# Kernel tuning notes

Measured on AMD Instinct MI355X. Metric: run time of the kernel, lower is better.

Reference implementation:

```python
import jax, jax.numpy as jnp
import numpy as np
from jax import lax

KS = 7  # kernel-prediction footprint at 1/4 res
DN = ('NCHW', 'OIHW', 'NCHW')


def _conv(x, W, b):
    y = lax.conv_general_dilated(x, W, (1, 1), 'VALID', dimension_numbers=DN)
    return y + b[None, :, None, None]


def _apply_kernels(kernel, data, ks):
    # kernel: [bs, ks*ks, kh, kw]; data: [bs, 1, h, w]
    kh, kw = kernel.shape[2], kernel.shape[3]
    h, w = data.shape[2], data.shape[3]
    ch = (h - (kh + ks - 1)) // 2
    cw = (w - (kw + ks - 1)) // 2
    if ch > 0:
        data = data[:, :, ch:h - ch, :]
    if cw > 0:
        data = data[:, :, :, cw:w - cw]
    # patches: [bs, ks*ks, kh, kw], flat tap index = dy*ks+dx (row-major), same as torch unfold+view
    patches = lax.conv_general_dilated_patches(data, (ks, ks), (1, 1), 'VALID')
    return jnp.sum(kernel * patches, axis=1, keepdims=True)


def _crop_like(a, b):
    dh = (a.shape[2] - b.shape[2]) // 2
    dw = (a.shape[3] - b.shape[3]) // 2
    if dh > 0 or dw > 0:
        a = a[:, :, dh:a.shape[2] - dh, dw:a.shape[3] - dw]
    return a


def _unroll(buf):
    # [bs,4,h,w] quarter-res -> [bs,1,2h,2w] full-res (channel c=2p+q -> offset (p,q))
    bs, _, h, w = buf.shape
    return buf.reshape(bs, 2, 2, h, w).transpose(0, 3, 1, 4, 2).reshape(bs, 1, 2 * h, 2 * w)


def reference(mosaic, W0, b0, W1, b1, W2, b2, W3, b3, W4, b4):
    gray = mosaic.sum(axis=1)  # [bs,H,W]
    # GRBG 2x2 phase extraction, matching torch unfold(2,2,2).unfold(1,2,2).permute(0,3,4,1,2)
    g0 = gray[:, 0::2, 0::2][:, None]
    b_ = gray[:, 1::2, 0::2][:, None]
    r = gray[:, 0::2, 1::2][:, None]
    g1 = gray[:, 1::2, 1::2][:, None]
    x = jnp.concatenate([g0, b_, r, g1], axis=1)  # [bs,4,h,w]

    # ConvChain: 5 valid 3x3 convs, relu on all but last (linear output)
    for (W, bb) in ((W0, b0), (W1, b1), (W2, b2), (W3, b3)):
        x = jax.nn.relu(_conv(x, W, bb))
    kernels = _conv(x, W4, b4)  # [bs, 10*KS*KS, kh, kw]

    k2 = KS * KS
    idx = 0

    reds = [r]
    for _ in range(3):
        k = jax.nn.softmax(kernels[:, idx:idx + k2], axis=1)
        idx += k2
        reds.append(_apply_kernels(k, r, KS))
    reds[0] = _crop_like(reds[0], reds[1])
    red = _unroll(jnp.concatenate([reds[1], reds[0], reds[2], reds[3]], axis=1))

    blues = [b_]
    for _ in range(3):
        k = jax.nn.softmax(kernels[:, idx:idx + k2], axis=1)
        idx += k2
        blues.append(_apply_kernels(k, b_, KS))
    blues[0] = _crop_like(blues[0], blues[1])
    blue = _unroll(jnp.concatenate([blues[1], blues[2], blues[0], blues[3]], axis=1))

    greens = [g0, g1]
    for _ in range(2):
        k = jax.nn.softmax(kernels[:, idx:idx + 2 * k2], axis=1)
        idx += 2 * k2
        greens.append(_apply_kernels(k[:, :k2], g0, KS) + _apply_kernels(k[:, k2:], g1, KS))
    greens[0] = _crop_like(greens[0], greens[2])
    greens[1] = _crop_like(greens[1], greens[2])
    green = _unroll(jnp.concatenate([greens[0], greens[2], greens[3], greens[1]], axis=1))

    return jnp.concatenate([red, green, blue], axis=1)  # [bs,3,2*kh,2*kw]


def setup_inputs() -> dict:
    key = jax.random.key(0)
    ks = jax.random.split(key, 6)
    bs, H, W = 2, 768, 768
    mosaic = jax.random.uniform(ks[0], (bs, 3, H, W), dtype=jnp.float32)

    def w(k, o, i):
        return jax.random.normal(k, (o, i, 3, 3), jnp.float32) * (1.0 / np.sqrt(i * 9))

    z = lambda n: jnp.zeros((n,), jnp.float32)
    return {
        'mosaic': mosaic,
        'W0': w(ks[1], 64, 4), 'b0': z(64),
        'W1': w(ks[2], 64, 64), 'b1': z(64),
        'W2': w(ks[3], 64, 64), 'b2': z(64),
        'W3': w(ks[4], 64, 64), 'b3': z(64),
        'W4': w(ks[5], 490, 64), 'b4': z(490),
    }
```

## Files before the change

### kernel.cpp

```cpp
#include <hip/hip_runtime.h>
#include <hip/hip_bf16.h>
#include <math.h>


typedef __attribute__((ext_vector_type(8))) short short8;
typedef __attribute__((ext_vector_type(4))) short short4v;
typedef __attribute__((ext_vector_type(4))) float f32x4;

static __device__ __forceinline__ short f2bf(float v) {
    __bf16 h = (__bf16)v;
    return __builtin_bit_cast(short, h);
}

__global__ __launch_bounds__(256) void split_k(const float* __restrict__ mosaic,
                                               float* __restrict__ x0) {
    int idx = blockIdx.x * 256 + threadIdx.x;
    const int total = 2 * 4 * 384 * 384;
    if (idx >= total) return;
    int x = idx % 384;
    int t = idx / 384;
    int y = t % 384;  t /= 384;
    int c = t % 4;
    int b = t / 4;
    int Y = 2 * y + ((c == 1 || c == 3) ? 1 : 0);
    int X = 2 * x + ((c == 2 || c == 3) ? 1 : 0);
    const float* mb = mosaic + (size_t)b * 3 * 768 * 768;
    float g = mb[Y * 768 + X] + mb[768 * 768 + Y * 768 + X] + mb[2 * 768 * 768 + Y * 768 + X];
    x0[idx] = g;
}

__global__ __launch_bounds__(256) void repack_k(const float* __restrict__ W,
                                                short* __restrict__ dst) {
    int idx = blockIdx.x * 256 + threadIdx.x;
    if (idx >= 9 * 64 * 64) return;
    int ic = idx % 64;
    int t2 = idx / 64;
    int oc = t2 % 64;
    int t  = t2 / 64;
    dst[idx] = f2bf(W[((size_t)oc * 64 + ic) * 9 + t]);
}

__global__ __launch_bounds__(256) void repack4_k(const float* __restrict__ W4,
                                                 const float* __restrict__ b4,
                                                 short* __restrict__ Wq,
                                                 float* __restrict__ bq) {
    int idx = blockIdx.x * 256 + threadIdx.x;
    if (idx < 9 * 640 * 64) {
        int ic  = idx % 64;
        int t2  = idx / 64;
        int ocn = t2 % 640;
        int tap = t2 / 640;
        int k  = ocn >> 6;
        int ql = ocn & 63;
        float v = (ql < 49) ? W4[((size_t)(49 * k + ql) * 64 + ic) * 9 + tap] : 0.f;
        Wq[idx] = f2bf(v);
    }
    if (idx < 640) {
        int k = idx >> 6, ql = idx & 63;
        bq[idx] = (ql < 49) ? b4[49 * k + ql] : 0.f;
    }
}

__global__ __launch_bounds__(256) void conv0_k(const float* __restrict__ x0f,
                                               const float* __restrict__ W0,
                                               const float* __restrict__ b0,
                                               short* __restrict__ out) {
    __shared__ float w[64 * 36];
    __shared__ float bb[64];
    for (int e = threadIdx.x; e < 64 * 36; e += 256) w[e] = W0[e];
    if (threadIdx.x < 64) bb[threadIdx.x] = b0[threadIdx.x];
    __syncthreads();
    int idx = blockIdx.x * 256 + threadIdx.x;
    if (idx >= 2 * 382 * 382) return;
    int x = idx % 382;
    int t = idx / 382;
    int y = t % 382;
    int b = t / 382;
    const float* base = x0f + (size_t)b * 4 * 384 * 384;
    float in[4][9];
#pragma unroll
    for (int ic = 0; ic < 4; ++ic)
#pragma unroll
        for (int ky = 0; ky < 3; ++ky)
#pragma unroll
            for (int kx = 0; kx < 3; ++kx)
                in[ic][ky * 3 + kx] = base[ic * 384 * 384 + (y + ky) * 384 + (x + kx)];
    short* op = out + (((size_t)b * 382 + y) * 382 + x) * 64;
    float accs[8];
    for (int og = 0; og < 8; ++og) {
#pragma unroll
        for (int oo = 0; oo < 8; ++oo) {
            int oc = og * 8 + oo;
            float acc = bb[oc];
            const float* wp = w + oc * 36;
#pragma unroll
            for (int ic = 0; ic < 4; ++ic)
#pragma unroll
                for (int e = 0; e < 9; ++e)
                    acc = fmaf(in[ic][e], wp[ic * 9 + e], acc);
            accs[oo] = fmaxf(acc, 0.f);
        }
        short8 pk;
#pragma unroll
        for (int oo = 0; oo < 8; ++oo) pk[oo] = f2bf(accs[oo]);
        *(short8*)(op + og * 8) = pk;
    }
}

template <int EPI>
__global__ __launch_bounds__(256, 2) void convp_k(
    const short* __restrict__ act,
    int Hin, int Hout, int YITER, int nstrips,
    const short* __restrict__ Wq,
    int CoutT,
    const float* __restrict__ bias,
    short* __restrict__ outbf,
    const float* __restrict__ x0f,
    float* __restrict__ out,
    float* __restrict__ pM, float* __restrict__ pD, float* __restrict__ pN) {
    const int tid = threadIdx.x;
    const int wave = tid >> 6;
    const int lane = tid & 63;
    const int wr = wave >> 1, wc = wave & 1;
    const int l15 = lane & 15, l4 = lane >> 4;

    const int q8 = gridDim.x >> 3;
    int L = ((int)blockIdx.x & 7) * q8 + ((int)blockIdx.x >> 3);
    int z = 0;
    if (EPI) { z = L % 10; L /= 10; }
    const int xt = L % 6; L /= 6;
    const int strip = L % nstrips;
    const int b = L / nstrips;
    const int x0c = xt * 64;
    const int y0 = strip * YITER;
    const int cnt = min(YITER, Hout - y0);
    if (cnt <= 0) return;

    __shared__ __align__(16) short Bt[8 * 528 * 8];
    __shared__ float smM[2][64], smD[2][64], smN[2][64];
    __shared__ float smP[17 * 72];

    auto stage_row = [&](int r) {
        const size_t rowbase = ((size_t)b * Hin + r) * (size_t)Hin;
        const int ring = (r & 7) * 528;
#pragma unroll
        for (int i = 0; i < 2; ++i) {
            int s = i * 256 + tid;
            int xl = s >> 3, sl = s & 7;
            int gx = x0c + xl; if (gx > Hin - 1) gx = Hin - 1;
            const short* src = act + (rowbase + gx) * 64 + ((sl ^ (xl & 7)) << 3);
            __builtin_amdgcn_global_load_lds(
                (const __attribute__((address_space(1))) void*)src,
                (__attribute__((address_space(3))) void*)((char*)Bt + (ring + s) * 16),
                16, 0, 0);
        }
        if (tid < 16) {
            int s = 512 + tid;
            int xl = s >> 3, sl = s & 7;
            int gx = x0c + xl; if (gx > Hin - 1) gx = Hin - 1;
            const short* src = act + (rowbase + gx) * 64 + ((sl ^ (xl & 7)) << 3);
            __builtin_amdgcn_global_load_lds(
                (const __attribute__((address_space(1))) void*)src,
                (__attribute__((address_space(3))) void*)((char*)Bt + (ring + s) * 16),
                16, 0, 0);
        }
    };

    const int zrow = EPI ? z * 64 : 0;
    short8 wreg[9][2][2];
#pragma unroll
    for (int tap = 0; tap < 9; ++tap)
#pragma unroll
        for (int kk = 0; kk < 2; ++kk)
#pragma unroll
            for (int m = 0; m < 2; ++m)
                wreg[tap][kk][m] = *(const short8*)(Wq +
                    ((size_t)tap * CoutT + zrow + wr * 32 + m * 16 + l15) * 64
                    + kk * 32 + l4 * 8);

    float bv[2][4];
    int goff[2][4];
    if (EPI) {
        int pidx = (z < 3) ? 2 : (z < 6) ? 1 : ((z & 1) ? 3 : 0);
        const float* plane = x0f + ((size_t)b * 4 + pidx) * 384 * 384;
#pragma unroll
        for (int m = 0; m < 2; ++m)
#pragma unroll
            for (int r = 0; r < 4; ++r) {
                int q = wr * 32 + m * 16 + l4 * 4 + r;
                bv[m][r] = (q < 49) ? bias[z * 64 + q] : -1e30f;
                int qc = (q < 49) ? q : 48;
                goff[m][r] = (qc / 7) * 72 + (qc % 7);
            }
        for (int e = tid; e < 17 * 70; e += 256) {
            int pr = e / 70, pc = e % 70;
            int gy = y0 + 2 + pr; if (gy > 383) gy = 383;
            int gx = x0c + 2 + pc; if (gx > 383) gx = 383;
            smP[pr * 72 + pc] = plane[gy * 384 + gx];
        }
    }

    stage_row(y0);
    stage_row(y0 + 1);
    stage_row(y0 + 2);
    stage_row(y0 + 3);
    stage_row(y0 + 4);
    asm volatile("s_waitcnt vmcnt(4) lgkmcnt(0)\n\ts_barrier" ::: "memory");

    for (int i = 0; i < cnt; ++i) {
        const int y = y0 + i;

        f32x4 acc[2][2] = {};
#pragma unroll
        for (int tap = 0; tap < 9; ++tap) {
            const int ky = tap / 3, kx = tap % 3;
            const int rbase = ((y + ky) & 7) * 528;
            short8 bf[2][2];
#pragma unroll
            for (int kk = 0; kk < 2; ++kk)
#pragma unroll
                for (int n = 0; n < 2; ++n) {
                    int xl = wc * 32 + n * 16 + l15 + kx;
                    int slot = (kk * 4 + l4) ^ (xl & 7);
                    bf[kk][n] = *(const short8*)&Bt[(rbase + xl * 8 + slot) * 8];
                }
#pragma unroll
            for (int kk = 0; kk < 2; ++kk)
#pragma unroll
                for (int m = 0; m < 2; ++m)
#pragma unroll
                    for (int n = 0; n < 2; ++n)
                        acc[m][n] = __builtin_amdgcn_mfma_f32_16x16x32_bf16(
                            wreg[tap][kk][m], bf[kk][n], acc[m][n], 0, 0, 0);
        }

        if (!EPI) {
#pragma unroll
            for (int m = 0; m < 2; ++m) {
                int ocb = wr * 32 + m * 16 + l4 * 4;
#pragma unroll
                for (int n = 0; n < 2; ++n) {
                    int x = x0c + wc * 32 + n * 16 + l15;
                    if (x >= Hout) continue;
                    size_t off = (((size_t)b * Hout + y) * Hout + x) * 64 + ocb;
                    short4v pk;
#pragma unroll
                    for (int r = 0; r < 4; ++r)
                        pk[r] = f2bf(fmaxf(acc[m][n][r] + bias[ocb + r], 0.f));
                    *(short4v*)(outbf + off) = pk;
                }
            }
        } else {
#pragma unroll
            for (int n = 0; n < 2; ++n) {
                const int xn = x0c + wc * 32 + n * 16 + l15;
                const int xg = (xn < 374) ? xn : 373;
                const int gbase = i * 72 + (xg - x0c);
                float mx = -1e30f;
#pragma unroll
                for (int m = 0; m < 2; ++m)
#pragma unroll
                    for (int r = 0; r < 4; ++r)
                        mx = fmaxf(mx, acc[m][n][r] + bv[m][r]);
                mx = fmaxf(mx, __shfl_xor(mx, 16));
                mx = fmaxf(mx, __shfl_xor(mx, 32));
                float den = 0.f, num = 0.f;
#pragma unroll
                for (int m = 0; m < 2; ++m)
#pragma unroll
                    for (int r = 0; r < 4; ++r) {
                        float e = __expf(acc[m][n][r] + bv[m][r] - mx);
                        den += e;
                        num = fmaf(e, smP[gbase + goff[m][r]], num);
                    }
                den += __shfl_xor(den, 16);  den += __shfl_xor(den, 32);
                num += __shfl_xor(num, 16);  num += __shfl_xor(num, 32);
                if (l4 == 0) {
                    int p = wc * 32 + n * 16 + l15;
                    smM[wr][p] = mx;
                    smD[wr][p] = den;
                    smN[wr][p] = num;
                }
            }
            asm volatile("s_waitcnt lgkmcnt(0)\n\ts_barrier" ::: "memory");
            if (tid < 64) {
                int p = tid, x = x0c + p;
                if (x < 374) {
                    float m0 = smM[0][p], m1 = smM[1][p];
                    float M = fmaxf(m0, m1);
                    float s0 = __expf(m0 - M), s1 = __expf(m1 - M);
                    float D = smD[0][p] * s0 + smD[1][p] * s1;
                    float N = smN[0][p] * s0 + smN[1][p] * s1;
                    if (z < 6) {
                        int color = (z < 3) ? 0 : 2;
                        int oy, ox;
                        switch (z) {
                            case 0: oy = 0; ox = 0; break;
                            case 1: oy = 1; ox = 0; break;
                            case 2: oy = 1; ox = 1; break;
                            case 3: oy = 0; ox = 0; break;
                            case 4: oy = 0; ox = 1; break;
                            default: oy = 1; ox = 1; break;
                        }
                        out[(((size_t)b * 3 + color) * 748 + 2 * y + oy) * 748 + 2 * x + ox] = N / D;
                    } else {
                        size_t po = (((size_t)(z - 6) * 2 + b) * 374 + y) * 374 + x;
                        pM[po] = M; pD[po] = D; pN[po] = N;
                    }
                }
            }
        }

        if (i <= cnt - 4) stage_row(y + 5);
        asm volatile("s_waitcnt vmcnt(4) lgkmcnt(0)\n\ts_barrier" ::: "memory");
    }
}

__global__ __launch_bounds__(256) void rawcomb_k(
    const float* __restrict__ x0f,
    const float* __restrict__ pM, const float* __restrict__ pD,
    const float* __restrict__ pN,
    float* __restrict__ out) {
    int idx = blockIdx.x * 256 + threadIdx.x;
    if (idx >= 2 * 374 * 374) return;
    int x = idx % 374;
    int t = idx / 374;
    int y = t % 374;
    int b = t / 374;
    const float* pb = x0f + (size_t)b * 4 * 384 * 384;
    float* ob = out + (size_t)b * 3 * 748 * 748;
    float g0v = pb[(y + 5) * 384 + x + 5];
    float blv = pb[384 * 384 + (y + 5) * 384 + x + 5];
    float rrv = pb[2 * 384 * 384 + (y + 5) * 384 + x + 5];
    float g1v = pb[3 * 384 * 384 + (y + 5) * 384 + x + 5];
    ob[((size_t)0 * 748 + 2 * y) * 748 + 2 * x + 1]     = rrv;
    ob[((size_t)2 * 748 + 2 * y + 1) * 748 + 2 * x]     = blv;
    ob[((size_t)1 * 748 + 2 * y) * 748 + 2 * x]         = g0v;
    ob[((size_t)1 * 748 + 2 * y + 1) * 748 + 2 * x + 1] = g1v;
#pragma unroll
    for (int g = 0; g < 2; ++g) {
        size_t o0 = (((size_t)(g * 2 + 0) * 2 + b) * 374 + y) * 374 + x;
        size_t o1 = (((size_t)(g * 2 + 1) * 2 + b) * 374 + y) * 374 + x;
        float m0 = pM[o0], m1 = pM[o1];
        float M = fmaxf(m0, m1);
        float s0 = __expf(m0 - M), s1 = __expf(m1 - M);
        float val = (pN[o0] * s0 + pN[o1] * s1) / (pD[o0] * s0 + pD[o1] * s1);
        int oy = g ? 1 : 0, ox = g ? 0 : 1;
        ob[((size_t)1 * 748 + 2 * y + oy) * 748 + 2 * x + ox] = val;
    }
}

extern "C" void kernel_launch(void* const* d_in, const int* in_sizes, int n_in,
                              void* d_out, int out_size, void* d_ws, size_t ws_size,
                              hipStream_t stream) {
    const float* mosaic = (const float*)d_in[0];
    const float* W0 = (const float*)d_in[1];  const float* b0 = (const float*)d_in[2];
    const float* W1 = (const float*)d_in[3];  const float* b1 = (const float*)d_in[4];
    const float* W2 = (const float*)d_in[5];  const float* b2 = (const float*)d_in[6];
    const float* W3 = (const float*)d_in[7];  const float* b3 = (const float*)d_in[8];
    const float* W4 = (const float*)d_in[9];  const float* b4 = (const float*)d_in[10];
    float* out = (float*)d_out;

    char* ws = (char*)d_ws;
    float* x0f    = (float*)ws;  ws += 4718592;
    short* Wq1    = (short*)ws;  ws += 73728;
    short* Wq2    = (short*)ws;  ws += 73728;
    short* Wq3    = (short*)ws;  ws += 73728;
    short* Wq4p   = (short*)ws;  ws += 737280;
    float* bias4p = (float*)ws;  ws += 2560;
    short* bufA   = (short*)ws;  ws += 37356544;
    short* bufB   = (short*)ws;  ws += 36966400;
    float* pM     = (float*)ws;  ws += 4477568;
    float* pD     = (float*)ws;  ws += 4477568;
    float* pN     = (float*)ws;

    split_k<<<(2 * 4 * 384 * 384 + 255) / 256, 256, 0, stream>>>(mosaic, x0f);

    repack_k<<<(9 * 64 * 64 + 255) / 256, 256, 0, stream>>>(W1, Wq1);
    repack_k<<<(9 * 64 * 64 + 255) / 256, 256, 0, stream>>>(W2, Wq2);
    repack_k<<<(9 * 64 * 64 + 255) / 256, 256, 0, stream>>>(W3, Wq3);
    repack4_k<<<(9 * 640 * 64 + 255) / 256, 256, 0, stream>>>(W4, b4, Wq4p, bias4p);

    conv0_k<<<(2 * 382 * 382 + 255) / 256, 256, 0, stream>>>(x0f, W0, b0, bufA);

    convp_k<0><<<456, 256, 0, stream>>>(bufA, 382, 380, 10, 38, Wq1, 64, b1,
                                        bufB, nullptr, nullptr, nullptr, nullptr, nullptr);
    convp_k<0><<<456, 256, 0, stream>>>(bufB, 380, 378, 10, 38, Wq2, 64, b2,
                                        bufA, nullptr, nullptr, nullptr, nullptr, nullptr);
    convp_k<0><<<456, 256, 0, stream>>>(bufA, 378, 376, 10, 38, Wq3, 64, b3,
                                        bufB, nullptr, nullptr, nullptr, nullptr, nullptr);

    convp_k<1><<<4080, 256, 0, stream>>>(bufB, 376, 374, 11, 34, Wq4p, 640, bias4p,
                                         nullptr, x0f, out, pM, pD, pN);

    rawcomb_k<<<(2 * 374 * 374 + 255) / 256, 256, 0, stream>>>(x0f, pM, pD, pN, out);
}
```

Before: 435.5 us.

## Shrink LDS ring and patch tile, fold bias into accumulators, raise MFMA priority

The LDS row ring drops from 8 to 6 slots and the patch tile is stored as bf16, which cuts shared memory per block so more blocks can be resident. The strip height goes from 10/11 to 8 rows, with more blocks launched to match. The bias now initialises the accumulators instead of being added in the epilogue, and the MFMA loop runs at raised wave priority. The tail iterations now drain all outstanding loads. The risks are bf16 rounding of the input plane in the kernel-application sum, and more halo reloads from the shorter strips.

Result: slower. 504.1 us (+15.8%).

```diff
diff --git a/kernel.cpp b/kernel.cpp
--- a/kernel.cpp
+++ b/kernel.cpp
@@ -10,6 +10,10 @@
 static __device__ __forceinline__ short f2bf(float v) {
     __bf16 h = (__bf16)v;
     return __builtin_bit_cast(short, h);
+}
+static __device__ __forceinline__ float bf2f(short s) {
+    unsigned u = ((unsigned)(unsigned short)s) << 16;
+    return __builtin_bit_cast(float, u);
 }
 
 __global__ __launch_bounds__(256) void split_k(const float* __restrict__ mosaic,
@@ -136,13 +140,13 @@
     const int cnt = min(YITER, Hout - y0);
     if (cnt <= 0) return;
 
-    __shared__ __align__(16) short Bt[8 * 528 * 8];
+    __shared__ __align__(16) short Bt[6 * 528 * 8];
     __shared__ float smM[2][64], smD[2][64], smN[2][64];
-    __shared__ float smP[17 * 72];
+    __shared__ short smP[14 * 72];
 
     auto stage_row = [&](int r) {
         const size_t rowbase = ((size_t)b * Hin + r) * (size_t)Hin;
-        const int ring = (r & 7) * 528;
+        const int ring = (r % 6) * 528;
 #pragma unroll
         for (int i = 0; i < 2; ++i) {
             int s = i * 256 + tid;
@@ -178,7 +182,7 @@
                     ((size_t)tap * CoutT + zrow + wr * 32 + m * 16 + l15) * 64
                     + kk * 32 + l4 * 8);
 
-    float bv[2][4];
+    float iv[2][4];
     int goff[2][4];
     if (EPI) {
         int pidx = (z < 3) ? 2 : (z < 6) ? 1 : ((z & 1) ? 3 : 0);
@@ -188,16 +192,22 @@
 #pragma unroll
             for (int r = 0; r < 4; ++r) {
                 int q = wr * 32 + m * 16 + l4 * 4 + r;
-                bv[m][r] = (q < 49) ? bias[z * 64 + q] : -1e30f;
+                iv[m][r] = (q < 49) ? bias[z * 64 + q] : -1e30f;
                 int qc = (q < 49) ? q : 48;
                 goff[m][r] = (qc / 7) * 72 + (qc % 7);
             }
-        for (int e = tid; e < 17 * 70; e += 256) {
+        for (int e = tid; e < 14 * 70; e += 256) {
             int pr = e / 70, pc = e % 70;
             int gy = y0 + 2 + pr; if (gy > 383) gy = 383;
             int gx = x0c + 2 + pc; if (gx > 383) gx = 383;
-            smP[pr * 72 + pc] = plane[gy * 384 + gx];
-        }
+            smP[pr * 72 + pc] = f2bf(plane[gy * 384 + gx]);
+        }
+    } else {
+#pragma unroll
+        for (int m = 0; m < 2; ++m)
+#pragma unroll
+            for (int r = 0; r < 4; ++r)
+                iv[m][r] = bias[wr * 32 + m * 16 + l4 * 4 + r];
     }
 
     stage_row(y0);
@@ -210,11 +220,20 @@
     for (int i = 0; i < cnt; ++i) {
         const int y = y0 + i;
 
-        f32x4 acc[2][2] = {};
+        f32x4 acc[2][2];
+#pragma unroll
+        for (int m = 0; m < 2; ++m)
+#pragma unroll
+            for (int n = 0; n < 2; ++n) {
+                acc[m][n][0] = iv[m][0]; acc[m][n][1] = iv[m][1];
+                acc[m][n][2] = iv[m][2]; acc[m][n][3] = iv[m][3];
+            }
+
+        __builtin_amdgcn_s_setprio(1);
 #pragma unroll
         for (int tap = 0; tap < 9; ++tap) {
             const int ky = tap / 3, kx = tap % 3;
-            const int rbase = ((y + ky) & 7) * 528;
+            const int rbase = ((y + ky) % 6) * 528;
             short8 bf[2][2];
 #pragma unroll
             for (int kk = 0; kk < 2; ++kk)
@@ -233,6 +252,7 @@
                         acc[m][n] = __builtin_amdgcn_mfma_f32_16x16x32_bf16(
                             wreg[tap][kk][m], bf[kk][n], acc[m][n], 0, 0, 0);
         }
+        __builtin_amdgcn_s_setprio(0);
 
         if (!EPI) {
 #pragma unroll
@@ -246,7 +266,7 @@
                     short4v pk;
 #pragma unroll
                     for (int r = 0; r < 4; ++r)
-                        pk[r] = f2bf(fmaxf(acc[m][n][r] + bias[ocb + r], 0.f));
+                        pk[r] = f2bf(fmaxf(acc[m][n][r], 0.f));
                     *(short4v*)(outbf + off) = pk;
                 }
             }
@@ -261,7 +281,7 @@
                 for (int m = 0; m < 2; ++m)
 #pragma unroll
                     for (int r = 0; r < 4; ++r)
-                        mx = fmaxf(mx, acc[m][n][r] + bv[m][r]);
+                        mx = fmaxf(mx, acc[m][n][r]);
                 mx = fmaxf(mx, __shfl_xor(mx, 16));
                 mx = fmaxf(mx, __shfl_xor(mx, 32));
                 float den = 0.f, num = 0.f;
@@ -269,9 +289,9 @@
                 for (int m = 0; m < 2; ++m)
 #pragma unroll
                     for (int r = 0; r < 4; ++r) {
-                        float e = __expf(acc[m][n][r] + bv[m][r] - mx);
+                        float e = __expf(acc[m][n][r] - mx);
                         den += e;
-                        num = fmaf(e, smP[gbase + goff[m][r]], num);
+                        num = fmaf(e, bf2f(smP[gbase + goff[m][r]]), num);
                     }
                 den += __shfl_xor(den, 16);  den += __shfl_xor(den, 32);
                 num += __shfl_xor(num, 16);  num += __shfl_xor(num, 32);
@@ -311,8 +331,12 @@
             }
         }
 
-        if (i <= cnt - 4) stage_row(y + 5);
-        asm volatile("s_waitcnt vmcnt(4) lgkmcnt(0)\n\ts_barrier" ::: "memory");
+        if (i <= cnt - 4) {
+            stage_row(y + 5);
+            asm volatile("s_waitcnt vmcnt(4) lgkmcnt(0)\n\ts_barrier" ::: "memory");
+        } else {
+            asm volatile("s_waitcnt vmcnt(0) lgkmcnt(0)\n\ts_barrier" ::: "memory");
+        }
     }
 }
 
@@ -383,14 +407,14 @@
 
     conv0_k<<<(2 * 382 * 382 + 255) / 256, 256, 0, stream>>>(x0f, W0, b0, bufA);
 
-    convp_k<0><<<456, 256, 0, stream>>>(bufA, 382, 380, 10, 38, Wq1, 64, b1,
+    convp_k<0><<<576, 256, 0, stream>>>(bufA, 382, 380, 8, 48, Wq1, 64, b1,
                                         bufB, nullptr, nullptr, nullptr, nullptr, nullptr);
-    convp_k<0><<<456, 256, 0, stream>>>(bufB, 380, 378, 10, 38, Wq2, 64, b2,
+    convp_k<0><<<576, 256, 0, stream>>>(bufB, 380, 378, 8, 48, Wq2, 64, b2,
                                         bufA, nullptr, nullptr, nullptr, nullptr, nullptr);
-    convp_k<0><<<456, 256, 0, stream>>>(bufA, 378, 376, 10, 38, Wq3, 64, b3,
+    convp_k<0><<<576, 256, 0, stream>>>(bufA, 378, 376, 8, 48, Wq3, 64, b3,
                                         bufB, nullptr, nullptr, nullptr, nullptr, nullptr);
 
-    convp_k<1><<<4080, 256, 0, stream>>>(bufB, 376, 374, 11, 34, Wq4p, 640, bias4p,
+    convp_k<1><<<5640, 256, 0, stream>>>(bufB, 376, 374, 8, 47, Wq4p, 640, bias4p,
                                          nullptr, x0f, out, pM, pD, pN);
 
     rawcomb_k<<<(2 * 374 * 374 + 255) / 256, 256, 0, stream>>>(x0f, pM, pD, pN, out);
```
